# Performance work log

Measured on AMD Instinct MI355X. Metric: run time of the kernel, lower is better.

The kernel has to match this reference:

```python
import jax, jax.numpy as jnp
import numpy as np

B, N, D, H = 128, 512, 128, 8
DH = D // H
CLIP = 10.0          # tanh_clipping
NEG = -1.0e9         # finite -inf for masking (keeps grads clean)


def setup_inputs() -> dict:
    key = jax.random.key(0)
    ks = jax.random.split(key, 6)
    s = 0.08  # ~1/sqrt(D) init scale so pre-tanh logits are in a sane range
    return {
        "embeddings": jax.random.normal(ks[0], (B, N, D), jnp.float32),
        "W_node_proj": jax.random.normal(ks[1], (D, 3 * D), jnp.float32) * s,
        "W_fixed_ctx": jax.random.normal(ks[2], (D, D), jnp.float32) * s,
        "W_step_ctx": jax.random.normal(ks[3], (2 * D, D), jnp.float32) * s,
        "W_out": jax.random.normal(ks[4], (D, D), jnp.float32) * s,
        "W_placeholder": jax.random.uniform(ks[5], (2 * D,), jnp.float32, -1.0, 1.0),
    }


def reference(embeddings, W_node_proj, W_fixed_ctx, W_step_ctx, W_out, W_placeholder):
    # _precompute: fixed context + glimpse K/V + logit key (cached for all steps)
    graph_embed = embeddings.mean(axis=1)                    # [B,D]
    fixed_ctx = graph_embed @ W_fixed_ctx                    # [B,D]
    proj = embeddings @ W_node_proj                          # [B,N,3D]
    gK, gV, logit_K = jnp.split(proj, 3, axis=-1)
    gK = gK.reshape(B, N, H, DH)                             # glimpse key heads
    gV = gV.reshape(B, N, H, DH)                             # glimpse val heads
    inv_sqrt_dh = 1.0 / jnp.sqrt(jnp.float32(DH))
    inv_sqrt_d = 1.0 / jnp.sqrt(jnp.float32(D))
    batch_idx = jnp.arange(B)

    def step(carry, _):
        visited, first, prev, i = carry
        # step context: placeholder at i==0, else concat(first, current) embeddings
        cur_ctx = jnp.concatenate(
            [embeddings[batch_idx, first], embeddings[batch_idx, prev]], axis=-1)  # [B,2D]
        step_ctx = jnp.where(i == 0, W_placeholder[None, :], cur_ctx)
        q = fixed_ctx + step_ctx @ W_step_ctx                # [B,D]
        qh = q.reshape(B, H, DH)
        # masked multi-head glimpse attention
        compat = jnp.einsum('bhd,bnhd->bhn', qh, gK) * inv_sqrt_dh
        compat = jnp.where(visited[:, None, :], NEG, compat)
        attn = jax.nn.softmax(compat, axis=-1)
        heads = jnp.einsum('bhn,bnhd->bhd', attn, gV)
        glimpse = heads.reshape(B, D) @ W_out                # project_out
        # logit attention with tanh clipping
        logits = jnp.einsum('bd,bnd->bn', glimpse, logit_K) * inv_sqrt_d
        logits = CLIP * jnp.tanh(logits)
        logits = jnp.where(visited, NEG, logits)
        log_p = jax.nn.log_softmax(logits, axis=-1)
        sel = jnp.argmax(log_p, axis=-1).astype(jnp.int32)   # greedy decode
        visited = visited.at[batch_idx, sel].set(True)
        first = jnp.where(i == 0, sel, first)
        return (visited, first, sel, i + 1), (log_p, sel)

    init = (jnp.zeros((B, N), bool), jnp.zeros((B,), jnp.int32),
            jnp.zeros((B,), jnp.int32), jnp.int32(0))
    _, (log_ps, pis) = jax.lax.scan(step, init, None, length=N)
    log_p = jnp.transpose(log_ps, (1, 0, 2))                 # [B,N_steps,N]
    pi = jnp.transpose(pis, (1, 0))                          # [B,N_steps]
    # _calc_log_likelihood
    ll = jnp.take_along_axis(log_p, pi[:, :, None], axis=2).squeeze(-1).sum(axis=1)
    return log_p, pi, ll
```

## Files before the change

### kernel.cpp

```cpp
#include <hip/hip_runtime.h>
#include <hip/hip_bf16.h>
#include <math.h>

#define BATCH 128
#define NN 512
#define DD 128
#define D3 384
#define NEGV (-1.0e9f)
#define NEGINF (-1.0e30f)

__global__ __launch_bounds__(256) void k_fixed(const float* __restrict__ emb,
                                               const float* __restrict__ Wf,
                                               const float* __restrict__ Wstep,
                                               const float* __restrict__ Wph,
                                               float* __restrict__ fixedc,
                                               float* __restrict__ q0) {
  const int b = blockIdx.x;
  __shared__ float s_part[2][DD];
  __shared__ float s_ge[DD];
  const int tid = threadIdx.x;
  const int d = tid & 127, c = tid >> 7;
  const float* e = emb + (size_t)b * NN * DD;
  float acc = 0.f;
  for (int n = c * 256; n < c * 256 + 256; ++n) acc += e[(size_t)n * DD + d];
  s_part[c][d] = acc;
  __syncthreads();
  if (tid < DD) s_ge[tid] = (s_part[0][tid] + s_part[1][tid]) * (1.0f / 512.0f);
  __syncthreads();
  if (tid < DD) {
    float a = 0.f;
    for (int k = 0; k < DD; ++k) a += s_ge[k] * Wf[k * DD + tid];
    fixedc[b * DD + tid] = a;
    float pq = 0.f;
    for (int k = 0; k < 2 * DD; ++k) pq += Wph[k] * Wstep[k * DD + tid];
    q0[b * DD + tid] = a + pq;
  }
}

__global__ __launch_bounds__(384) void k_proj(const float* __restrict__ emb,
                                              const float* __restrict__ Wp,
                                              float* __restrict__ proj) {
  const size_t row0 = (size_t)blockIdx.x * 32;
  __shared__ float s_A[32][DD];
  const int tid = threadIdx.x;
  for (int t = tid; t < 32 * DD; t += 384)
    s_A[t >> 7][t & 127] = emb[row0 * DD + t];
  __syncthreads();
  float acc[32];
#pragma unroll
  for (int r = 0; r < 32; ++r) acc[r] = 0.f;
  const int c = tid;
  for (int k = 0; k < DD; ++k) {
    float w = Wp[k * D3 + c];
#pragma unroll
    for (int r = 0; r < 32; ++r) acc[r] += s_A[r][k] * w;
  }
  for (int r = 0; r < 32; ++r) proj[(row0 + r) * D3 + c] = acc[r];
}

__global__ __launch_bounds__(128) void k_lp(float* __restrict__ proj,
                                            const float* __restrict__ Wout) {
  const size_t row0 = (size_t)blockIdx.x * 32;
  __shared__ float s_L[32][DD];
  const int tid = threadIdx.x;
  for (int rr = 0; rr < 32; ++rr)
    s_L[rr][tid] = proj[(row0 + rr) * D3 + 2 * DD + tid];
  __syncthreads();
  float acc[32];
#pragma unroll
  for (int r = 0; r < 32; ++r) acc[r] = 0.f;
  for (int d = 0; d < DD; ++d) {
    const float w = Wout[tid * DD + d];
#pragma unroll
    for (int r = 0; r < 32; ++r) acc[r] += w * s_L[r][d];
  }
  for (int r = 0; r < 32; ++r)
    proj[(row0 + r) * D3 + 2 * DD + tid] = acc[r];
}

__global__ __launch_bounds__(256) void k_ectx(const float* __restrict__ emb,
                                              const float* __restrict__ Wstep,
                                              const float* __restrict__ fixedc,
                                              float* __restrict__ E12) {
  const size_t row0 = (size_t)blockIdx.x * 32;
  __shared__ float s_A[32][DD];
  const int tid = threadIdx.x;
  for (int t = tid; t < 32 * DD; t += 256)
    s_A[t >> 7][t & 127] = emb[row0 * DD + t];
  __syncthreads();
  float acc[32];
#pragma unroll
  for (int r = 0; r < 32; ++r) acc[r] = 0.f;
  const int c = tid;
  const int b = (int)(row0 >> 9);
  const float* wp = (c < DD) ? (Wstep + c) : (Wstep + DD * DD + (c - DD));
  for (int k = 0; k < DD; ++k) {
    float w = wp[(size_t)k * DD];
#pragma unroll
    for (int r = 0; r < 32; ++r) acc[r] += s_A[r][k] * w;
  }
  const float fc = (c < DD) ? fixedc[b * DD + c] : 0.f;
  for (int r = 0; r < 32; ++r) E12[(row0 + r) * 256 + c] = acc[r] + fc;
}

#define DOT16(q, F)                                                           \
  (q[0] * F[0].x + q[1] * F[0].y + q[2] * F[0].z + q[3] * F[0].w +            \
   q[4] * F[1].x + q[5] * F[1].y + q[6] * F[1].z + q[7] * F[1].w +            \
   q[8] * F[2].x + q[9] * F[2].y + q[10] * F[2].z + q[11] * F[2].w +          \
   q[12] * F[3].x + q[13] * F[3].y + q[14] * F[3].z + q[15] * F[3].w)

#define L_LOAD(njx, Lr)                                                       \
  {                                                                           \
    const float4* lp_ =                                                       \
        (const float4*)(projb + (size_t)(njx)*D3 + 2 * DD + h * 16);          \
    Lr[0] = lp_[0]; Lr[1] = lp_[1]; Lr[2] = lp_[2]; Lr[3] = lp_[3];           \
  }

#define L_CONSUME(Lr, njx)                                                    \
  {                                                                           \
    float a_ = DOT16(gf, Lr);                                                 \
    a_ += __shfl_xor(a_, 1);                                                  \
    a_ += __shfl_xor(a_, 2);                                                  \
    a_ += __shfl_xor(a_, 4);                                                  \
    if (h == 0) {                                                             \
      const float lg_ = 10.0f * tanhf(a_ * inv_sqrt_d);                       \
      s_logits[njx] = lg_;                                                    \
      asum += expf(lg_);                                                      \
      if (lg_ > av || (lg_ == av && (njx) < ai)) { av = lg_; ai = (njx); }    \
    }                                                                         \
  }

__global__ __launch_bounds__(1024, 1) void k_decode(
    const float* __restrict__ emb, const float* __restrict__ proj,
    const float* __restrict__ fixedc, const float* __restrict__ q0,
    const float* __restrict__ E12, const float* __restrict__ Wstep,
    const float* __restrict__ Wph, const int useE, float* __restrict__ out) {
  const int b = blockIdx.x;
  const int tid = threadIdx.x;
  const int lane = tid & 63;
  const int wave = tid >> 6;
  const int h = tid & 7, r = tid >> 3;

  __shared__ float4 s_Lpf[2][4][16][64];
  __shared__ int s_idx[NN];
  __shared__ int s_pos[NN];
  __shared__ unsigned char s_visited[NN];
  __shared__ float s_hacc[16][8][17];
  __shared__ float s_heads[DD];
  __shared__ float s_logits[NN];
  __shared__ float s_rm[16];
  __shared__ int s_ri[16];
  __shared__ float s_es[16];
  __shared__ float s_q[DD];
  __shared__ float s_ctx[2 * DD];
  __shared__ int s_first, s_prev, s_M, s_swap;
  __shared__ float s_ll;

  const float inv_sqrt_d = 0.08838834764831845f;
  const size_t eb = (size_t)b * NN * DD;
  const size_t e2 = (size_t)b * NN * 256;
  const float* projb = proj + (size_t)b * NN * D3;
  float* outp = out + (size_t)b * NN * NN;
  const size_t PI_OFF = (size_t)BATCH * NN * NN;
  const size_t LL_OFF = PI_OFF + (size_t)BATCH * NN;

  if (tid < NN) {
    s_idx[tid] = tid;
    s_pos[tid] = tid;
    s_visited[tid] = 0;
  }
  if (tid == 0) { s_first = 0; s_prev = 0; s_ll = 0.f; s_M = NN; }
#pragma unroll
  for (int s = 0; s < 2; ++s) {
    const float4* lp =
        (const float4*)(projb + (size_t)(r + s * 128) * D3 + 2 * DD + h * 16);
    s_Lpf[s][0][wave][lane] = lp[0];
    s_Lpf[s][1][wave][lane] = lp[1];
    s_Lpf[s][2][wave][lane] = lp[2];
    s_Lpf[s][3][wave][lane] = lp[3];
  }
  __syncthreads();

  for (int i = 0; i < NN; ++i) {
    const int M = s_M;
    const int first = s_first, prev = s_prev;

    float qf[16];
    if (useE) {
      if (i == 0) {
#pragma unroll
        for (int d = 0; d < 4; ++d) {
          const float4 v = *(const float4*)(q0 + b * DD + h * 16 + d * 4);
          qf[d * 4 + 0] = v.x; qf[d * 4 + 1] = v.y;
          qf[d * 4 + 2] = v.z; qf[d * 4 + 3] = v.w;
        }
      } else {
        const float* e1p = E12 + e2 + (size_t)first * 256 + h * 16;
        const float* e2p = E12 + e2 + (size_t)prev * 256 + DD + h * 16;
#pragma unroll
        for (int d = 0; d < 4; ++d) {
          const float4 a = *(const float4*)(e1p + d * 4);
          const float4 c = *(const float4*)(e2p + d * 4);
          qf[d * 4 + 0] = a.x + c.x;
          qf[d * 4 + 1] = a.y + c.y;
          qf[d * 4 + 2] = a.z + c.z;
          qf[d * 4 + 3] = a.w + c.w;
        }
      }
    } else {
      if (tid < 2 * DD) {
        float v;
        if (i == 0)
          v = Wph[tid];
        else
          v = (tid < DD) ? emb[eb + (size_t)first * DD + tid]
                         : emb[eb + (size_t)prev * DD + (tid - DD)];
        s_ctx[tid] = v;
      }
      __syncthreads();
      if (tid < DD) {
        float a = fixedc[b * DD + tid];
        for (int k = 0; k < 2 * DD; ++k) a += s_ctx[k] * Wstep[k * DD + tid];
        s_q[tid] = a;
      }
      __syncthreads();
#pragma unroll
      for (int d = 0; d < 16; ++d) qf[d] = s_q[h * 16 + d];
    }

    bool act[4];
    int nj[4];
#pragma unroll
    for (int k = 0; k < 4; ++k) {
      const int j = r + k * 128;
      act[k] = (j < M);
      nj[k] = s_idx[j];
    }
    float s_l = 0.f;
    float acc[16];
#pragma unroll
    for (int d = 0; d < 16; ++d) acc[d] = 0.f;
#pragma unroll
    for (int k = 0; k < 4; ++k) {
      if (act[k]) {
        const float* rp = projb + (size_t)nj[k] * D3 + h * 16;
        const float4* kp = (const float4*)rp;
        float4 k0 = kp[0], k1 = kp[1], k2 = kp[2], k3 = kp[3];
        float a = qf[0] * k0.x + qf[1] * k0.y + qf[2] * k0.z + qf[3] * k0.w +
                  qf[4] * k1.x + qf[5] * k1.y + qf[6] * k1.z + qf[7] * k1.w +
                  qf[8] * k2.x + qf[9] * k2.y + qf[10] * k2.z + qf[11] * k2.w +
                  qf[12] * k3.x + qf[13] * k3.y + qf[14] * k3.z +
                  qf[15] * k3.w;
        const float p = expf(a * 0.25f);
        s_l += p;
        const float4* vp = (const float4*)(rp + DD);
        float4 v0 = vp[0], v1 = vp[1], v2 = vp[2], v3 = vp[3];
        acc[0] += p * v0.x;  acc[1] += p * v0.y;
        acc[2] += p * v0.z;  acc[3] += p * v0.w;
        acc[4] += p * v1.x;  acc[5] += p * v1.y;
        acc[6] += p * v1.z;  acc[7] += p * v1.w;
        acc[8] += p * v2.x;  acc[9] += p * v2.y;
        acc[10] += p * v2.z; acc[11] += p * v2.w;
        acc[12] += p * v3.x; acc[13] += p * v3.y;
        acc[14] += p * v3.z; acc[15] += p * v3.w;
      }
    }
    {
      const bool k1 = (lane & 8) == 0;
#pragma unroll
      for (int d = 0; d < 8; ++d) {
        const float send = k1 ? acc[d + 8] : acc[d];
        const float got = __shfl_xor(send, 8);
        acc[d] = (k1 ? acc[d] : acc[d + 8]) + got;
      }
      const bool k2 = (lane & 16) == 0;
#pragma unroll
      for (int d = 0; d < 4; ++d) {
        const float send = k2 ? acc[d + 4] : acc[d];
        const float got = __shfl_xor(send, 16);
        acc[d] = (k2 ? acc[d] : acc[d + 4]) + got;
      }
      const bool k3 = (lane & 32) == 0;
#pragma unroll
      for (int d = 0; d < 2; ++d) {
        const float send = k3 ? acc[d + 2] : acc[d];
        const float got = __shfl_xor(send, 32);
        acc[d] = (k3 ? acc[d] : acc[d + 2]) + got;
      }
    }
    s_l += __shfl_xor(s_l, 8);
    s_l += __shfl_xor(s_l, 16);
    s_l += __shfl_xor(s_l, 32);
    {
      const int dim0 = ((lane & 8) ? 8 : 0) | ((lane & 16) ? 4 : 0) |
                       ((lane & 32) ? 2 : 0);
      s_hacc[wave][h][dim0] = acc[0];
      s_hacc[wave][h][dim0 + 1] = acc[1];
      if (lane < 8) s_hacc[wave][lane][16] = s_l;
    }
    if (tid >= 512) {
      const int t2 = tid - 512;
      if (s_visited[t2]) s_logits[t2] = NEGV;
    }
    __syncthreads();

    if (tid < DD) {
      const int hh = tid >> 4, dh = tid & 15;
      float num = 0.f, den = 0.f;
#pragma unroll
      for (int w = 0; w < 16; ++w) {
        num += s_hacc[w][hh][dh];
        den += s_hacc[w][hh][16];
      }
      s_heads[tid] = num / den;
    }
    __syncthreads();

    float gf[16];
#pragma unroll
    for (int d = 0; d < 16; ++d) gf[d] = s_heads[h * 16 + d];
    float av = NEGINF;
    int ai = 0x7FFFFFFF;
    float asum = 0.f;
    if (act[0]) {
      float4 LA[4];
      LA[0] = s_Lpf[0][0][wave][lane];
      LA[1] = s_Lpf[0][1][wave][lane];
      LA[2] = s_Lpf[0][2][wave][lane];
      LA[3] = s_Lpf[0][3][wave][lane];
      L_CONSUME(LA, nj[0]);
    }
    if (act[1]) {
      float4 LA[4];
      LA[0] = s_Lpf[1][0][wave][lane];
      LA[1] = s_Lpf[1][1][wave][lane];
      LA[2] = s_Lpf[1][2][wave][lane];
      LA[3] = s_Lpf[1][3][wave][lane];
      L_CONSUME(LA, nj[1]);
    }
    if (act[2]) {
      float4 LA[4];
      L_LOAD(nj[2], LA);
      L_CONSUME(LA, nj[2]);
    }
    if (act[3]) {
      float4 LA[4];
      L_LOAD(nj[3], LA);
      L_CONSUME(LA, nj[3]);
    }
#pragma unroll
    for (int off = 1; off <= 32; off <<= 1) {
      const float ov = __shfl_xor(av, off);
      const int oi = __shfl_xor(ai, off);
      asum += __shfl_xor(asum, off);
      if (ov > av || (ov == av && oi < ai)) { av = ov; ai = oi; }
    }
    if (lane == 0) { s_rm[wave] = av; s_ri[wave] = ai; s_es[wave] = asum; }
    __syncthreads();

    float bv = s_rm[0];
    int bi = s_ri[0];
    float bs = s_es[0];
#pragma unroll
    for (int w2 = 1; w2 < 16; ++w2) {
      const float ov = s_rm[w2];
      const int oi = s_ri[w2];
      bs += s_es[w2];
      if (ov > bv || (ov == bv && oi < bi)) { bv = ov; bi = oi; }
    }
    const float lz = logf(bs);
    const int sel = bi;
    if (tid < NN) outp[(size_t)i * NN + tid] = s_logits[tid] - lz;
    if (tid == 0) {
      s_ll += s_logits[sel] - lz;
      s_visited[sel] = 1;
      if (i == 0) s_first = sel;
      s_prev = sel;
      out[PI_OFF + (size_t)b * NN + i] = (float)sel;
      const int p = s_pos[sel];
      const int last = s_idx[M - 1];
      s_idx[p] = last;
      s_pos[last] = p;
      s_idx[M - 1] = sel;
      s_pos[sel] = M - 1;
      s_M = M - 1;
      s_swap = p;
    }
    __syncthreads();

    {
      const int sp = s_swap;
      if (sp < 256 && r == (sp & 127)) {
        const int sl = sp >> 7;
        const int nr = s_idx[sp];
        const float4* lp =
            (const float4*)(projb + (size_t)nr * D3 + 2 * DD + h * 16);
        s_Lpf[sl][0][wave][lane] = lp[0];
        s_Lpf[sl][1][wave][lane] = lp[1];
        s_Lpf[sl][2][wave][lane] = lp[2];
        s_Lpf[sl][3][wave][lane] = lp[3];
      }
    }
  }
  if (tid == 0) out[LL_OFF + b] = s_ll;
}

extern "C" void kernel_launch(void* const* d_in, const int* in_sizes, int n_in,
                              void* d_out, int out_size, void* d_ws,
                              size_t ws_size, hipStream_t stream) {
  const float* emb = (const float*)d_in[0];
  const float* Wnp = (const float*)d_in[1];
  const float* Wf = (const float*)d_in[2];
  const float* Wstep = (const float*)d_in[3];
  const float* Wout = (const float*)d_in[4];
  const float* Wph = (const float*)d_in[5];
  float* out = (float*)d_out;

  const size_t projN = (size_t)BATCH * NN * D3;
  const size_t eN = (size_t)BATCH * NN * 256;
  const size_t need_full = (projN + eN + 2 * (size_t)BATCH * DD) * 4;

  float* proj = (float*)d_ws;
  float* E12 = proj + projN;
  const int useE = (ws_size >= need_full) ? 1 : 0;
  float* fixedc = useE ? (E12 + eN) : (proj + projN);
  float* q0 = fixedc + (size_t)BATCH * DD;

  k_fixed<<<BATCH, 256, 0, stream>>>(emb, Wf, Wstep, Wph, fixedc, q0);
  k_proj<<<(BATCH * NN) / 32, 384, 0, stream>>>(emb, Wnp, proj);
  k_lp<<<(BATCH * NN) / 32, 128, 0, stream>>>(proj, Wout);
  if (useE) k_ectx<<<(BATCH * NN) / 32, 256, 0, stream>>>(emb, Wstep, fixedc, E12);
  k_decode<<<BATCH, 1024, 0, stream>>>(emb, proj, fixedc, q0,
                                       useE ? E12 : nullptr, Wstep, Wph, useE,
                                       out);
}
```

Measured before the change: 5.802 ms.

## Prefetch logit keys early and reduce argmax with wave shuffles

The global loads of the logit-key rows for the third and fourth node chunks are now issued before the heads-reduction barrier, so their latency overlaps the head combine instead of stalling inside the logit loop. The visited-mask write is moved to the phase after that barrier. The final cross-wave argmax and sum reduction now runs as a shuffle reduction in wave 0 instead of every thread looping serially over 16 partials, and the log_p row store is moved after the swap barrier using a shared lz value. This adds register pressure from the 32 extra float registers held across barriers.

```diff
diff --git a/kernel.cpp b/kernel.cpp
--- a/kernel.cpp
+++ b/kernel.cpp
@@ -154,7 +154,7 @@
   __shared__ float s_q[DD];
   __shared__ float s_ctx[2 * DD];
   __shared__ int s_first, s_prev, s_M, s_swap;
-  __shared__ float s_ll;
+  __shared__ float s_ll, s_lzv;
 
   const float inv_sqrt_d = 0.08838834764831845f;
   const size_t eb = (size_t)b * NN * DD;
@@ -298,9 +298,13 @@
       s_hacc[wave][h][dim0 + 1] = acc[1];
       if (lane < 8) s_hacc[wave][lane][16] = s_l;
     }
-    if (tid >= 512) {
-      const int t2 = tid - 512;
-      if (s_visited[t2]) s_logits[t2] = NEGV;
+    float4 Lf2[4], Lf3[4];
+    {
+      const int j2 = r + 256, j3 = r + 384;
+      const int nj2p = s_idx[(j2 < M) ? j2 : (M - 1)];
+      const int nj3p = s_idx[(j3 < M) ? j3 : (M - 1)];
+      L_LOAD(nj2p, Lf2);
+      L_LOAD(nj3p, Lf3);
     }
     __syncthreads();
 
@@ -313,6 +317,9 @@
         den += s_hacc[w][hh][16];
       }
       s_heads[tid] = num / den;
+    } else if (tid >= 512) {
+      const int t2 = tid - 512;
+      if (s_visited[t2]) s_logits[t2] = NEGV;
     }
     __syncthreads();
 
@@ -338,16 +345,8 @@
       LA[3] = s_Lpf[1][3][wave][lane];
       L_CONSUME(LA, nj[1]);
     }
-    if (act[2]) {
-      float4 LA[4];
-      L_LOAD(nj[2], LA);
-      L_CONSUME(LA, nj[2]);
-    }
-    if (act[3]) {
-      float4 LA[4];
-      L_LOAD(nj[3], LA);
-      L_CONSUME(LA, nj[3]);
-    }
+    if (act[2]) { L_CONSUME(Lf2, nj[2]); }
+    if (act[3]) { L_CONSUME(Lf3, nj[3]); }
 #pragma unroll
     for (int off = 1; off <= 32; off <<= 1) {
       const float ov = __shfl_xor(av, off);
@@ -358,33 +357,35 @@
     if (lane == 0) { s_rm[wave] = av; s_ri[wave] = ai; s_es[wave] = asum; }
     __syncthreads();
 
-    float bv = s_rm[0];
-    int bi = s_ri[0];
-    float bs = s_es[0];
-#pragma unroll
-    for (int w2 = 1; w2 < 16; ++w2) {
-      const float ov = s_rm[w2];
-      const int oi = s_ri[w2];
-      bs += s_es[w2];
-      if (ov > bv || (ov == bv && oi < bi)) { bv = ov; bi = oi; }
-    }
-    const float lz = logf(bs);
-    const int sel = bi;
-    if (tid < NN) outp[(size_t)i * NN + tid] = s_logits[tid] - lz;
-    if (tid == 0) {
-      s_ll += s_logits[sel] - lz;
-      s_visited[sel] = 1;
-      if (i == 0) s_first = sel;
-      s_prev = sel;
-      out[PI_OFF + (size_t)b * NN + i] = (float)sel;
-      const int p = s_pos[sel];
-      const int last = s_idx[M - 1];
-      s_idx[p] = last;
-      s_pos[last] = p;
-      s_idx[M - 1] = sel;
-      s_pos[sel] = M - 1;
-      s_M = M - 1;
-      s_swap = p;
+    if (wave == 0) {
+      float cv = (lane < 16) ? s_rm[lane] : NEGINF;
+      int ci = (lane < 16) ? s_ri[lane] : 0x7FFFFFFF;
+      float cs = (lane < 16) ? s_es[lane] : 0.f;
+#pragma unroll
+      for (int off = 1; off <= 8; off <<= 1) {
+        const float ov = __shfl_xor(cv, off);
+        const int oi = __shfl_xor(ci, off);
+        cs += __shfl_xor(cs, off);
+        if (ov > cv || (ov == cv && oi < ci)) { cv = ov; ci = oi; }
+      }
+      if (lane == 0) {
+        const float lzv = logf(cs);
+        const int sel = ci;
+        s_lzv = lzv;
+        s_ll += s_logits[sel] - lzv;
+        s_visited[sel] = 1;
+        if (i == 0) s_first = sel;
+        s_prev = sel;
+        out[PI_OFF + (size_t)b * NN + i] = (float)sel;
+        const int p = s_pos[sel];
+        const int last = s_idx[M - 1];
+        s_idx[p] = last;
+        s_pos[last] = p;
+        s_idx[M - 1] = sel;
+        s_pos[sel] = M - 1;
+        s_M = M - 1;
+        s_swap = p;
+      }
     }
     __syncthreads();
 
@@ -401,6 +402,8 @@
         s_Lpf[sl][3][wave][lane] = lp[3];
       }
     }
+    const float lz = s_lzv;
+    if (tid < NN) outp[(size_t)i * NN + tid] = s_logits[tid] - lz;
   }
   if (tid == 0) out[LL_OFF + b] = s_ll;
 }
```

Result: no change. 5.807 ms (+0.1%).
